# Kernel tuning notes

Measured on AMD Instinct MI355X. Metric: run time of the kernel, lower is better.

Reference implementation:

```python
import jax, jax.numpy as jnp
import numpy as np

CUTOFF = 5.2
BOX = 44.0
N_ATOMS = 8192

# 13 half-shifts used by the cell list (vector_index_displacement) + zero shift
HALF_SHIFTS = np.array([
    [-1, 0, 0], [-1, -1, 0], [0, -1, 0], [1, -1, 0],
    [-1, 1, -1], [0, 1, -1], [1, 1, -1], [-1, 0, -1],
    [0, 0, -1], [1, 0, -1], [-1, -1, -1], [0, -1, -1], [1, -1, -1]], dtype=np.int64)
ALL_SHIFTS = np.concatenate([np.zeros((1, 3), dtype=np.int64), HALF_SHIFTS], axis=0)  # (14,3)


def setup_inputs() -> dict:
    key = jax.random.key(0)
    k1, k2 = jax.random.split(key)
    species = jax.random.randint(k1, (1, N_ATOMS), 0, 4, dtype=jnp.int64)
    coordinates = jax.random.uniform(k2, (1, N_ATOMS, 3), dtype=jnp.float32) * BOX
    cell = jnp.eye(3, dtype=jnp.float32) * BOX
    pbc = jnp.ones((3,), dtype=bool)
    return {"species": species, "coordinates": coordinates, "cell": cell, "pbc": pbc}


def reference(species, coordinates, cell, pbc):
    # Single molecule, as asserted by the torch module.
    coords = coordinates[0]  # (N, 3)
    n = coords.shape[0]
    # map_to_central: wrap coordinates into the central cell
    frac = coords @ jnp.linalg.inv(cell)
    frac = frac - jnp.floor(frac)
    coords = frac @ cell
    # orthorhombic cell diagonal (norm of cell columns, as in _setup_variables)
    diag = jnp.linalg.norm(cell, axis=0)  # (3,)

    shifts = jnp.asarray(ALL_SHIFTS)
    pairs_list, shift_list = [], []
    cutoff2 = CUTOFF * CUTOFF
    for k in range(shifts.shape[0]):  # fixed small loop over 14 periodic shifts
        s = shifts[k]
        # delta[i, j] = r_i - r_j + s * cell_diagonal   (N, N, 3)
        delta = coords[:, None, :] - coords[None, :, :] + s.astype(coords.dtype) * diag
        d2 = jnp.sum(delta * delta, axis=-1)  # (N, N)
        mask = d2 <= cutoff2
        if k == 0:
            # within-image pairs: each unordered pair once, no self pairs
            mask = jnp.triu(mask, 1)
        i, j = jnp.nonzero(mask)  # eager: data-dependent pair count
        pairs_list.append(jnp.stack([i, j], axis=0))
        shift_list.append(jnp.broadcast_to(s, (i.shape[0], 3)))
    atom_pairs = jnp.concatenate(pairs_list, axis=1)  # (2, P)
    shift_indices = jnp.concatenate(shift_list, axis=0)  # (P, 3)
    return atom_pairs, shift_indices


if __name__ == "__main__":
    out = reference(**setup_inputs())
    print(out[0].shape, out[1].shape)
```

## Files before the change

kernel.cpp:

```cpp
#include <hip/hip_runtime.h>

#define CLD_NATOMS 8192
#define CLD_NSHIFT 14
#define CLD_NROWS (CLD_NSHIFT * CLD_NATOMS)
#define CLD_NTILE 112
#define CLD_NCELL 512
#define CLD_CAP 128
#define CLD_C2 ((float)(5.2 * 5.2))
#define CLD_R 5.35f

__device__ const int cld_shifts[CLD_NSHIFT][3] = {
    {0, 0, 0},
    {-1, 0, 0}, {-1, -1, 0}, {0, -1, 0}, {1, -1, 0},
    {-1, 1, -1}, {0, 1, -1}, {1, 1, -1}, {-1, 0, -1},
    {0, 0, -1}, {1, 0, -1}, {-1, -1, -1}, {0, -1, -1}, {1, -1, -1}};

__device__ float4 cld_pp[CLD_NATOMS];
__device__ int cld_cid[CLD_NATOMS];
__device__ float4 cld_sorted[CLD_NATOMS];
__device__ unsigned cld_cstart[CLD_NCELL + 1];
__device__ unsigned cld_cfill[CLD_NCELL];
__device__ int cld_jbuf[(size_t)CLD_NROWS * CLD_CAP];
__device__ unsigned cld_cnt[CLD_NROWS];
__device__ unsigned cld_off[CLD_NROWS];
__device__ unsigned cld_tot[CLD_NTILE];
__device__ float4 cld_dg;
__device__ float4 cld_cinv;
__device__ float4 cld_sf[CLD_NSHIFT];

__global__ __launch_bounds__(256) void cld_wrapbin(const float* __restrict__ coords,
                                                   const float* __restrict__ cell) {
  int i = blockIdx.x * blockDim.x + threadIdx.x;
  if (i >= CLD_NATOMS) return;
  float dgx = (float)sqrt((double)cell[0] * cell[0] + (double)cell[3] * cell[3] +
                          (double)cell[6] * cell[6]);
  float dgy = (float)sqrt((double)cell[1] * cell[1] + (double)cell[4] * cell[4] +
                          (double)cell[7] * cell[7]);
  float dgz = (float)sqrt((double)cell[2] * cell[2] + (double)cell[5] * cell[5] +
                          (double)cell[8] * cell[8]);
  float cix = 8.0f / dgx, ciy = 8.0f / dgy, ciz = 8.0f / dgz;
  if (i == 0) {
    cld_dg = make_float4(dgx, dgy, dgz, 0.f);
    cld_cinv = make_float4(cix, ciy, ciz, 0.f);
    for (int k = 0; k < CLD_NSHIFT; ++k)
      cld_sf[k] = make_float4(__fmul_rn((float)cld_shifts[k][0], dgx),
                              __fmul_rn((float)cld_shifts[k][1], dgy),
                              __fmul_rn((float)cld_shifts[k][2], dgz), 0.f);
  }

  double a00 = cell[0], a01 = cell[1], a02 = cell[2];
  double a10 = cell[3], a11 = cell[4], a12 = cell[5];
  double a20 = cell[6], a21 = cell[7], a22 = cell[8];
  double det = a00 * (a11 * a22 - a12 * a21) - a01 * (a10 * a22 - a12 * a20) +
               a02 * (a10 * a21 - a11 * a20);
  double id = 1.0 / det;
  float inv[3][3];
  inv[0][0] = (float)((a11 * a22 - a12 * a21) * id);
  inv[0][1] = (float)(-(a01 * a22 - a02 * a21) * id);
  inv[0][2] = (float)((a01 * a12 - a02 * a11) * id);
  inv[1][0] = (float)(-(a10 * a22 - a12 * a20) * id);
  inv[1][1] = (float)((a00 * a22 - a02 * a20) * id);
  inv[1][2] = (float)(-(a00 * a12 - a02 * a10) * id);
  inv[2][0] = (float)((a10 * a21 - a11 * a20) * id);
  inv[2][1] = (float)(-(a00 * a21 - a01 * a20) * id);
  inv[2][2] = (float)((a00 * a11 - a01 * a10) * id);

  float x = coords[3 * i], y = coords[3 * i + 1], z = coords[3 * i + 2];
  float fr[3], w[3];
#pragma unroll
  for (int c = 0; c < 3; ++c) {
    float f = __fadd_rn(__fadd_rn(__fmul_rn(x, inv[0][c]), __fmul_rn(y, inv[1][c])),
                        __fmul_rn(z, inv[2][c]));
    fr[c] = __fsub_rn(f, floorf(f));
  }
#pragma unroll
  for (int c = 0; c < 3; ++c) {
    w[c] = __fadd_rn(
        __fadd_rn(__fmul_rn(fr[0], cell[0 * 3 + c]), __fmul_rn(fr[1], cell[1 * 3 + c])),
        __fmul_rn(fr[2], cell[2 * 3 + c]));
  }
  cld_pp[i] = make_float4(w[0], w[1], w[2], 0.0f);
  int cx = min(7, (int)(w[0] * cix));
  int cy = min(7, (int)(w[1] * ciy));
  int cz = min(7, (int)(w[2] * ciz));
  cld_cid[i] = (cz * 8 + cy) * 8 + cx;
}

__global__ __launch_bounds__(1024) void cld_cscan() {
  __shared__ unsigned h[CLD_NCELL];
  int t = threadIdx.x;
  if (t < CLD_NCELL) h[t] = 0u;
  __syncthreads();
#pragma unroll
  for (int r = 0; r < 8; ++r) atomicAdd(&h[cld_cid[t + r * 1024]], 1u);
  __syncthreads();
  unsigned v = (t < CLD_NCELL) ? h[t] : 0u;
  unsigned acc = v;
  for (int off = 1; off < CLD_NCELL; off <<= 1) {
    unsigned a = (t >= off && t < CLD_NCELL) ? h[t - off] : 0u;
    __syncthreads();
    if (t < CLD_NCELL) {
      acc += a;
      h[t] = acc;
    }
    __syncthreads();
  }
  if (t < CLD_NCELL) {
    cld_cstart[t] = acc - v;
    cld_cfill[t] = acc - v;
  }
  if (t == CLD_NCELL - 1) cld_cstart[CLD_NCELL] = acc;
}

__global__ __launch_bounds__(256) void cld_scatter() {
  int i = blockIdx.x * blockDim.x + threadIdx.x;
  if (i >= CLD_NATOMS) return;
  unsigned pos = atomicAdd(&cld_cfill[cld_cid[i]], 1u);
  float4 p = cld_pp[i];
  p.w = __int_as_float(i);
  cld_sorted[pos] = p;
}

__device__ __forceinline__ bool cld_alive(float xi, float yi, float zi, int sx, int sy,
                                          int sz, float dgx, float dgy, float dgz) {
  bool a = true;
  if (sx < 0) a = a && (xi >= dgx - 5.3f); else if (sx > 0) a = a && (xi <= 5.3f);
  if (sy < 0) a = a && (yi >= dgy - 5.3f); else if (sy > 0) a = a && (yi <= 5.3f);
  if (sz < 0) a = a && (zi >= dgz - 5.3f); else if (sz > 0) a = a && (zi <= 5.3f);
  return a;
}

__device__ __forceinline__ void cld_crange(float t, float ci, int& lo, int& hi) {
  lo = max(0, (int)(fmaxf(t - CLD_R, 0.f) * ci));
  hi = min(7, (int)(fmaxf(t + CLD_R, 0.f) * ci));
}

__device__ __forceinline__ unsigned cld_iscan(unsigned v, int lane) {
  for (int off = 1; off < 64; off <<= 1) {
    unsigned t = __shfl_up(v, off);
    if (lane >= off) v += t;
  }
  return v;
}

__global__ __launch_bounds__(512) void cld_count() {
  __shared__ uint4 smask[8][64];
  int wslot = threadIdx.x >> 6;
  int wv = blockIdx.x * 8 + wslot;
  int lane = threadIdx.x & 63;
  unsigned* lm = (unsigned*)smask[wslot];
  int k = wv >> 13, i = wv & (CLD_NATOMS - 1);

  float4 dg = cld_dg;
  float4 sc = cld_sf[k];
  int sx = cld_shifts[k][0], sy = cld_shifts[k][1], sz = cld_shifts[k][2];
  float4 pi = cld_pp[i];
  if (k != 0 && !cld_alive(pi.x, pi.y, pi.z, sx, sy, sz, dg.x, dg.y, dg.z)) {
    if (lane == 0) cld_cnt[wv] = 0u;
    return;
  }
  smask[wslot][lane] = make_uint4(0u, 0u, 0u, 0u);

  float4 cinv = cld_cinv;
  int xlo, xhi, ylo, yhi, zlo, zhi;
  cld_crange(__fadd_rn(pi.x, sc.x), cinv.x, xlo, xhi);
  cld_crange(__fadd_rn(pi.y, sc.y), cinv.y, ylo, yhi);
  cld_crange(__fadd_rn(pi.z, sc.z), cinv.z, zlo, zhi);

  for (int cz = zlo; cz <= zhi; ++cz) {
    for (int cy = ylo; cy <= yhi; ++cy) {
      int idb = (cz * 8 + cy) * 8;
      unsigned b = cld_cstart[idb + xlo], e = cld_cstart[idb + xhi + 1];
      for (unsigned t = b + lane; t < e; t += 64) {
        float4 pj = cld_sorted[t];
        int j = __float_as_int(pj.w);
        float dx = __fadd_rn(__fsub_rn(pi.x, pj.x), sc.x);
        float dy = __fadd_rn(__fsub_rn(pi.y, pj.y), sc.y);
        float dz = __fadd_rn(__fsub_rn(pi.z, pj.z), sc.z);
        float d2 = __fadd_rn(__fadd_rn(__fmul_rn(dx, dx), __fmul_rn(dy, dy)),
                             __fmul_rn(dz, dz));
        bool ok = (d2 <= CLD_C2) && (k != 0 || i < j);
        if (ok) atomicOr(&lm[(unsigned)j >> 5], 1u << (j & 31));
      }
    }
  }
  __threadfence_block();

  const unsigned long long* mrow = (const unsigned long long*)lm;
  unsigned long long m0 = mrow[lane];
  unsigned long long m1 = mrow[64 + lane];
  unsigned c0 = (unsigned)__popcll(m0), c1 = (unsigned)__popcll(m1);
  unsigned s0 = cld_iscan(c0, lane);
  unsigned T0 = __shfl(s0, 63);
  unsigned e0 = s0 - c0;
  unsigned s1 = cld_iscan(c1, lane);
  unsigned T1 = __shfl(s1, 63);
  unsigned e1 = T0 + s1 - c1;

  size_t jb = (size_t)wv * CLD_CAP;
  unsigned p = e0;
  unsigned long long m = m0;
  while (m) {
    int b = __ffsll((long long)m) - 1;
    m &= m - 1;
    if (p < CLD_CAP) cld_jbuf[jb + p] = (lane << 6) + b;
    ++p;
  }
  p = e1;
  m = m1;
  while (m) {
    int b = __ffsll((long long)m) - 1;
    m &= m - 1;
    if (p < CLD_CAP) cld_jbuf[jb + p] = ((64 + lane) << 6) + b;
    ++p;
  }
  if (lane == 0) cld_cnt[wv] = min(T0 + T1, (unsigned)CLD_CAP);
}

__global__ __launch_bounds__(1024) void cld_s1() {
  __shared__ unsigned sd[1024];
  int t = threadIdx.x;
  int gid = blockIdx.x * 1024 + t;
  unsigned v = cld_cnt[gid];
  sd[t] = v;
  __syncthreads();
  unsigned acc = v;
  for (int off = 1; off < 1024; off <<= 1) {
    unsigned a = (t >= off) ? sd[t - off] : 0u;
    __syncthreads();
    acc += a;
    sd[t] = acc;
    __syncthreads();
  }
  cld_off[gid] = acc - v;
  if (t == 1023) cld_tot[blockIdx.x] = acc;
}

__global__ __launch_bounds__(512) void cld_emit(int* __restrict__ out, int P) {
  int wv = blockIdx.x * 8 + (threadIdx.x >> 6);
  int lane = threadIdx.x & 63;
  unsigned c = cld_cnt[wv];
  if (c == 0) return;
  int tile = wv >> 10;
  unsigned v = 0;
  if (lane < tile) v = cld_tot[lane];
  if (64 + lane < tile) v += cld_tot[64 + lane];
#pragma unroll
  for (int off = 32; off; off >>= 1) v += __shfl_down(v, off);
  unsigned tbase = __shfl(v, 0);

  unsigned off0 = cld_off[wv] + tbase;
  int k = wv >> 13, i = wv & (CLD_NATOMS - 1);
  int sx = cld_shifts[k][0], sy = cld_shifts[k][1], sz = cld_shifts[k][2];
  size_t jb = (size_t)wv * CLD_CAP;
  for (unsigned q = lane; q < c; q += 64) {
    unsigned p = off0 + q;
    if (p < (unsigned)P) {
      out[p] = i;
      out[P + p] = cld_jbuf[jb + q];
      unsigned sp = 2u * (unsigned)P + 3u * p;
      out[sp] = sx;
      out[sp + 1] = sy;
      out[sp + 2] = sz;
    }
  }
}

extern "C" void kernel_launch(void* const* d_in, const int* in_sizes, int n_in,
                              void* d_out, int out_size, void* d_ws, size_t ws_size,
                              hipStream_t stream) {
  const float* coords = (const float*)d_in[1];
  const float* cell = (const float*)d_in[2];
  int P = out_size / 5;

  cld_wrapbin<<<CLD_NATOMS / 256, 256, 0, stream>>>(coords, cell);
  cld_cscan<<<1, 1024, 0, stream>>>();
  cld_scatter<<<CLD_NATOMS / 256, 256, 0, stream>>>();
  cld_count<<<CLD_NROWS / 8, 512, 0, stream>>>();
  cld_s1<<<CLD_NTILE, 1024, 0, stream>>>();
  cld_emit<<<CLD_NROWS / 8, 512, 0, stream>>>((int*)d_out, P);
}
```

Measured before the change: 53.24 us.

## Fuse count, scan and emit into one decoupled-lookback kernel and merge cell scan with scatter

Reduces the six-launch pipeline to three. The cell histogram/scan now runs in block 0 of the scatter kernel while the other blocks spin on a flag. Count, offset scan and emit are merged into one kernel that handles 128 rows per block and obtains its global base by spinning on earlier tiles' published totals. This removes launch gaps and the global cnt/off round trips, but relies on all earlier blocks making forward progress, and the serial lookback over up to 896 tiles adds latency.

```diff
diff --git a/kernel.cpp b/kernel.cpp
--- a/kernel.cpp
+++ b/kernel.cpp
@@ -1,37 +1,62 @@
 #include <hip/hip_runtime.h>
 
-#define CLD_NATOMS 8192
-#define CLD_NSHIFT 14
-#define CLD_NROWS (CLD_NSHIFT * CLD_NATOMS)
-#define CLD_NTILE 112
-#define CLD_NCELL 512
-#define CLD_CAP 128
-#define CLD_C2 ((float)(5.2 * 5.2))
-#define CLD_R 5.35f
-
-__device__ const int cld_shifts[CLD_NSHIFT][3] = {
+#define CLH_NATOMS 8192
+#define CLH_NSHIFT 14
+#define CLH_NROWS (CLH_NSHIFT * CLH_NATOMS)
+#define CLH_NCELL 512
+#define CLH_CAP 128
+#define CLH_TROWS 128
+#define CLH_NTILE (CLH_NROWS / CLH_TROWS)
+#define CLH_C2 ((float)(5.2 * 5.2))
+#define CLH_R 5.35f
+
+__device__ const int clh_shifts[CLH_NSHIFT][3] = {
     {0, 0, 0},
     {-1, 0, 0}, {-1, -1, 0}, {0, -1, 0}, {1, -1, 0},
     {-1, 1, -1}, {0, 1, -1}, {1, 1, -1}, {-1, 0, -1},
     {0, 0, -1}, {1, 0, -1}, {-1, -1, -1}, {0, -1, -1}, {1, -1, -1}};
 
-__device__ float4 cld_pp[CLD_NATOMS];
-__device__ int cld_cid[CLD_NATOMS];
-__device__ float4 cld_sorted[CLD_NATOMS];
-__device__ unsigned cld_cstart[CLD_NCELL + 1];
-__device__ unsigned cld_cfill[CLD_NCELL];
-__device__ int cld_jbuf[(size_t)CLD_NROWS * CLD_CAP];
-__device__ unsigned cld_cnt[CLD_NROWS];
-__device__ unsigned cld_off[CLD_NROWS];
-__device__ unsigned cld_tot[CLD_NTILE];
-__device__ float4 cld_dg;
-__device__ float4 cld_cinv;
-__device__ float4 cld_sf[CLD_NSHIFT];
-
-__global__ __launch_bounds__(256) void cld_wrapbin(const float* __restrict__ coords,
+__device__ float4 clh_pp[CLH_NATOMS];
+__device__ int clh_cid[CLH_NATOMS];
+__device__ float4 clh_sorted[CLH_NATOMS];
+__device__ unsigned clh_cstart[CLH_NCELL + 1];
+__device__ unsigned clh_cfill[CLH_NCELL];
+__device__ unsigned clh_flag;
+__device__ unsigned long long clh_tstat[CLH_NTILE];
+__device__ int clh_jbuf[(size_t)CLH_NROWS * CLH_CAP];
+__device__ float4 clh_dg;
+__device__ float4 clh_cinv;
+__device__ float4 clh_sf[CLH_NSHIFT];
+
+__device__ __forceinline__ bool clh_alive(float xi, float yi, float zi, int sx, int sy,
+                                          int sz, float dgx, float dgy, float dgz) {
+  bool a = true;
+  if (sx < 0) a = a && (xi >= dgx - 5.3f); else if (sx > 0) a = a && (xi <= 5.3f);
+  if (sy < 0) a = a && (yi >= dgy - 5.3f); else if (sy > 0) a = a && (yi <= 5.3f);
+  if (sz < 0) a = a && (zi >= dgz - 5.3f); else if (sz > 0) a = a && (zi <= 5.3f);
+  return a;
+}
+
+__device__ __forceinline__ void clh_crange(float t, float ci, int& lo, int& hi) {
+  lo = max(0, (int)(fmaxf(t - CLH_R, 0.f) * ci));
+  hi = min(7, (int)(fmaxf(t + CLH_R, 0.f) * ci));
+}
+
+__device__ __forceinline__ unsigned clh_iscan(unsigned v, int lane) {
+  for (int off = 1; off < 64; off <<= 1) {
+    unsigned t = __shfl_up(v, off);
+    if (lane >= off) v += t;
+  }
+  return v;
+}
+
+__global__ __launch_bounds__(256) void clh_wrapbin(const float* __restrict__ coords,
                                                    const float* __restrict__ cell) {
   int i = blockIdx.x * blockDim.x + threadIdx.x;
-  if (i >= CLD_NATOMS) return;
+  if (i >= CLH_NATOMS) return;
+  if (i < CLH_NTILE) clh_tstat[i] = 0ull;
+  if (i == 0) clh_flag = 0u;
+
   float dgx = (float)sqrt((double)cell[0] * cell[0] + (double)cell[3] * cell[3] +
                           (double)cell[6] * cell[6]);
   float dgy = (float)sqrt((double)cell[1] * cell[1] + (double)cell[4] * cell[4] +
@@ -40,12 +65,12 @@
                           (double)cell[8] * cell[8]);
   float cix = 8.0f / dgx, ciy = 8.0f / dgy, ciz = 8.0f / dgz;
   if (i == 0) {
-    cld_dg = make_float4(dgx, dgy, dgz, 0.f);
-    cld_cinv = make_float4(cix, ciy, ciz, 0.f);
-    for (int k = 0; k < CLD_NSHIFT; ++k)
-      cld_sf[k] = make_float4(__fmul_rn((float)cld_shifts[k][0], dgx),
-                              __fmul_rn((float)cld_shifts[k][1], dgy),
-                              __fmul_rn((float)cld_shifts[k][2], dgz), 0.f);
+    clh_dg = make_float4(dgx, dgy, dgz, 0.f);
+    clh_cinv = make_float4(cix, ciy, ciz, 0.f);
+    for (int k = 0; k < CLH_NSHIFT; ++k)
+      clh_sf[k] = make_float4(__fmul_rn((float)clh_shifts[k][0], dgx),
+                              __fmul_rn((float)clh_shifts[k][1], dgy),
+                              __fmul_rn((float)clh_shifts[k][2], dgz), 0.f);
   }
 
   double a00 = cell[0], a01 = cell[1], a02 = cell[2];
@@ -79,189 +104,188 @@
         __fadd_rn(__fmul_rn(fr[0], cell[0 * 3 + c]), __fmul_rn(fr[1], cell[1 * 3 + c])),
         __fmul_rn(fr[2], cell[2 * 3 + c]));
   }
-  cld_pp[i] = make_float4(w[0], w[1], w[2], 0.0f);
+  clh_pp[i] = make_float4(w[0], w[1], w[2], 0.0f);
   int cx = min(7, (int)(w[0] * cix));
   int cy = min(7, (int)(w[1] * ciy));
   int cz = min(7, (int)(w[2] * ciz));
-  cld_cid[i] = (cz * 8 + cy) * 8 + cx;
-}
-
-__global__ __launch_bounds__(1024) void cld_cscan() {
-  __shared__ unsigned h[CLD_NCELL];
-  int t = threadIdx.x;
-  if (t < CLD_NCELL) h[t] = 0u;
+  clh_cid[i] = (cz * 8 + cy) * 8 + cx;
+}
+
+__global__ __launch_bounds__(512) void clh_scatterfused() {
+  __shared__ unsigned h[CLH_NCELL];
+  int tid = threadIdx.x;
+  if (blockIdx.x == 0) {
+    h[tid] = 0u;
+    __syncthreads();
+    for (int r = tid; r < CLH_NATOMS; r += 512) atomicAdd(&h[clh_cid[r]], 1u);
+    __syncthreads();
+    unsigned v = h[tid];
+    unsigned acc = v;
+    for (int off = 1; off < CLH_NCELL; off <<= 1) {
+      unsigned a = (tid >= off) ? h[tid - off] : 0u;
+      __syncthreads();
+      acc += a;
+      h[tid] = acc;
+      __syncthreads();
+    }
+    clh_cstart[tid] = acc - v;
+    atomicExch(&clh_cfill[tid], acc - v);
+    if (tid == CLH_NCELL - 1) clh_cstart[CLH_NCELL] = acc;
+    __threadfence();
+    __syncthreads();
+    if (tid == 0) atomicExch(&clh_flag, 1u);
+  } else {
+    if (tid == 0) {
+      while (atomicAdd(&clh_flag, 0u) == 0u) __builtin_amdgcn_s_sleep(8);
+    }
+    __syncthreads();
+    __threadfence();
+  }
+  int i = blockIdx.x * 512 + tid;
+  float4 p = clh_pp[i];
+  unsigned pos = atomicAdd(&clh_cfill[clh_cid[i]], 1u);
+  p.w = __int_as_float(i);
+  clh_sorted[pos] = p;
+}
+
+__global__ __launch_bounds__(512) void clh_mega(int* __restrict__ out, int P) {
+  __shared__ uint4 smask[8][64];
+  __shared__ unsigned scnt[CLH_TROWS];
+  __shared__ unsigned soff[CLH_TROWS];
+  __shared__ unsigned sbase;
+  int tid = threadIdx.x;
+  int wslot = tid >> 6;
+  int lane = tid & 63;
+  unsigned* lm = (unsigned*)smask[wslot];
+
+  float4 dg = clh_dg;
+  float4 cinv = clh_cinv;
+
+  for (int r = 0; r < CLH_TROWS / 8; ++r) {
+    int local = wslot * (CLH_TROWS / 8) + r;
+    int row = blockIdx.x * CLH_TROWS + local;
+    int k = row >> 13, i = row & (CLH_NATOMS - 1);
+    int sx = clh_shifts[k][0], sy = clh_shifts[k][1], sz = clh_shifts[k][2];
+    float4 pi = clh_pp[i];
+    if (k != 0 && !clh_alive(pi.x, pi.y, pi.z, sx, sy, sz, dg.x, dg.y, dg.z)) {
+      if (lane == 0) scnt[local] = 0u;
+      continue;
+    }
+    float4 sc = clh_sf[k];
+    smask[wslot][lane] = make_uint4(0u, 0u, 0u, 0u);
+
+    int xlo, xhi, ylo, yhi, zlo, zhi;
+    clh_crange(__fadd_rn(pi.x, sc.x), cinv.x, xlo, xhi);
+    clh_crange(__fadd_rn(pi.y, sc.y), cinv.y, ylo, yhi);
+    clh_crange(__fadd_rn(pi.z, sc.z), cinv.z, zlo, zhi);
+
+    for (int cz = zlo; cz <= zhi; ++cz) {
+      for (int cy = ylo; cy <= yhi; ++cy) {
+        int idb = (cz * 8 + cy) * 8;
+        unsigned b = clh_cstart[idb + xlo], e = clh_cstart[idb + xhi + 1];
+        for (unsigned t = b + lane; t < e; t += 64) {
+          float4 pj = clh_sorted[t];
+          int j = __float_as_int(pj.w);
+          float dx = __fadd_rn(__fsub_rn(pi.x, pj.x), sc.x);
+          float dy = __fadd_rn(__fsub_rn(pi.y, pj.y), sc.y);
+          float dz = __fadd_rn(__fsub_rn(pi.z, pj.z), sc.z);
+          float d2 = __fadd_rn(__fadd_rn(__fmul_rn(dx, dx), __fmul_rn(dy, dy)),
+                               __fmul_rn(dz, dz));
+          bool ok = (d2 <= CLH_C2) && (k != 0 || i < j);
+          if (ok) atomicOr(&lm[(unsigned)j >> 5], 1u << (j & 31));
+        }
+      }
+    }
+    __threadfence_block();
+
+    const unsigned long long* mrow = (const unsigned long long*)lm;
+    unsigned long long m0 = mrow[lane];
+    unsigned long long m1 = mrow[64 + lane];
+    if (__ballot((m0 | m1) != 0ull) == 0ull) {
+      if (lane == 0) scnt[local] = 0u;
+      continue;
+    }
+    unsigned c0 = (unsigned)__popcll(m0), c1 = (unsigned)__popcll(m1);
+    unsigned s0 = clh_iscan(c0, lane);
+    unsigned T0 = __shfl(s0, 63);
+    unsigned e0 = s0 - c0;
+    unsigned s1 = clh_iscan(c1, lane);
+    unsigned T1 = __shfl(s1, 63);
+    unsigned e1 = T0 + s1 - c1;
+
+    size_t jb = (size_t)row * CLH_CAP;
+    unsigned p = e0;
+    unsigned long long m = m0;
+    while (m) {
+      int b = __ffsll((long long)m) - 1;
+      m &= m - 1;
+      if (p < CLH_CAP) clh_jbuf[jb + p] = (lane << 6) + b;
+      ++p;
+    }
+    p = e1;
+    m = m1;
+    while (m) {
+      int b = __ffsll((long long)m) - 1;
+      m &= m - 1;
+      if (p < CLH_CAP) clh_jbuf[jb + p] = ((64 + lane) << 6) + b;
+      ++p;
+    }
+    if (lane == 0) scnt[local] = min(T0 + T1, (unsigned)CLH_CAP);
+  }
   __syncthreads();
-#pragma unroll
-  for (int r = 0; r < 8; ++r) atomicAdd(&h[cld_cid[t + r * 1024]], 1u);
-  __syncthreads();
-  unsigned v = (t < CLD_NCELL) ? h[t] : 0u;
-  unsigned acc = v;
-  for (int off = 1; off < CLD_NCELL; off <<= 1) {
-    unsigned a = (t >= off && t < CLD_NCELL) ? h[t - off] : 0u;
-    __syncthreads();
-    if (t < CLD_NCELL) {
-      acc += a;
-      h[t] = acc;
-    }
-    __syncthreads();
-  }
-  if (t < CLD_NCELL) {
-    cld_cstart[t] = acc - v;
-    cld_cfill[t] = acc - v;
-  }
-  if (t == CLD_NCELL - 1) cld_cstart[CLD_NCELL] = acc;
-}
-
-__global__ __launch_bounds__(256) void cld_scatter() {
-  int i = blockIdx.x * blockDim.x + threadIdx.x;
-  if (i >= CLD_NATOMS) return;
-  unsigned pos = atomicAdd(&cld_cfill[cld_cid[i]], 1u);
-  float4 p = cld_pp[i];
-  p.w = __int_as_float(i);
-  cld_sorted[pos] = p;
-}
-
-__device__ __forceinline__ bool cld_alive(float xi, float yi, float zi, int sx, int sy,
-                                          int sz, float dgx, float dgy, float dgz) {
-  bool a = true;
-  if (sx < 0) a = a && (xi >= dgx - 5.3f); else if (sx > 0) a = a && (xi <= 5.3f);
-  if (sy < 0) a = a && (yi >= dgy - 5.3f); else if (sy > 0) a = a && (yi <= 5.3f);
-  if (sz < 0) a = a && (zi >= dgz - 5.3f); else if (sz > 0) a = a && (zi <= 5.3f);
-  return a;
-}
-
-__device__ __forceinline__ void cld_crange(float t, float ci, int& lo, int& hi) {
-  lo = max(0, (int)(fmaxf(t - CLD_R, 0.f) * ci));
-  hi = min(7, (int)(fmaxf(t + CLD_R, 0.f) * ci));
-}
-
-__device__ __forceinline__ unsigned cld_iscan(unsigned v, int lane) {
-  for (int off = 1; off < 64; off <<= 1) {
-    unsigned t = __shfl_up(v, off);
-    if (lane >= off) v += t;
-  }
-  return v;
-}
-
-__global__ __launch_bounds__(512) void cld_count() {
-  __shared__ uint4 smask[8][64];
-  int wslot = threadIdx.x >> 6;
-  int wv = blockIdx.x * 8 + wslot;
-  int lane = threadIdx.x & 63;
-  unsigned* lm = (unsigned*)smask[wslot];
-  int k = wv >> 13, i = wv & (CLD_NATOMS - 1);
-
-  float4 dg = cld_dg;
-  float4 sc = cld_sf[k];
-  int sx = cld_shifts[k][0], sy = cld_shifts[k][1], sz = cld_shifts[k][2];
-  float4 pi = cld_pp[i];
-  if (k != 0 && !cld_alive(pi.x, pi.y, pi.z, sx, sy, sz, dg.x, dg.y, dg.z)) {
-    if (lane == 0) cld_cnt[wv] = 0u;
-    return;
-  }
-  smask[wslot][lane] = make_uint4(0u, 0u, 0u, 0u);
-
-  float4 cinv = cld_cinv;
-  int xlo, xhi, ylo, yhi, zlo, zhi;
-  cld_crange(__fadd_rn(pi.x, sc.x), cinv.x, xlo, xhi);
-  cld_crange(__fadd_rn(pi.y, sc.y), cinv.y, ylo, yhi);
-  cld_crange(__fadd_rn(pi.z, sc.z), cinv.z, zlo, zhi);
-
-  for (int cz = zlo; cz <= zhi; ++cz) {
-    for (int cy = ylo; cy <= yhi; ++cy) {
-      int idb = (cz * 8 + cy) * 8;
-      unsigned b = cld_cstart[idb + xlo], e = cld_cstart[idb + xhi + 1];
-      for (unsigned t = b + lane; t < e; t += 64) {
-        float4 pj = cld_sorted[t];
-        int j = __float_as_int(pj.w);
-        float dx = __fadd_rn(__fsub_rn(pi.x, pj.x), sc.x);
-        float dy = __fadd_rn(__fsub_rn(pi.y, pj.y), sc.y);
-        float dz = __fadd_rn(__fsub_rn(pi.z, pj.z), sc.z);
-        float d2 = __fadd_rn(__fadd_rn(__fmul_rn(dx, dx), __fmul_rn(dy, dy)),
-                             __fmul_rn(dz, dz));
-        bool ok = (d2 <= CLD_C2) && (k != 0 || i < j);
-        if (ok) atomicOr(&lm[(unsigned)j >> 5], 1u << (j & 31));
-      }
-    }
-  }
-  __threadfence_block();
-
-  const unsigned long long* mrow = (const unsigned long long*)lm;
-  unsigned long long m0 = mrow[lane];
-  unsigned long long m1 = mrow[64 + lane];
-  unsigned c0 = (unsigned)__popcll(m0), c1 = (unsigned)__popcll(m1);
-  unsigned s0 = cld_iscan(c0, lane);
-  unsigned T0 = __shfl(s0, 63);
-  unsigned e0 = s0 - c0;
-  unsigned s1 = cld_iscan(c1, lane);
-  unsigned T1 = __shfl(s1, 63);
-  unsigned e1 = T0 + s1 - c1;
-
-  size_t jb = (size_t)wv * CLD_CAP;
-  unsigned p = e0;
-  unsigned long long m = m0;
-  while (m) {
-    int b = __ffsll((long long)m) - 1;
-    m &= m - 1;
-    if (p < CLD_CAP) cld_jbuf[jb + p] = (lane << 6) + b;
-    ++p;
-  }
-  p = e1;
-  m = m1;
-  while (m) {
-    int b = __ffsll((long long)m) - 1;
-    m &= m - 1;
-    if (p < CLD_CAP) cld_jbuf[jb + p] = ((64 + lane) << 6) + b;
-    ++p;
-  }
-  if (lane == 0) cld_cnt[wv] = min(T0 + T1, (unsigned)CLD_CAP);
-}
-
-__global__ __launch_bounds__(1024) void cld_s1() {
-  __shared__ unsigned sd[1024];
-  int t = threadIdx.x;
-  int gid = blockIdx.x * 1024 + t;
-  unsigned v = cld_cnt[gid];
-  sd[t] = v;
+
+  unsigned v = (tid < CLH_TROWS) ? scnt[tid] : 0u;
+  if (tid < CLH_TROWS) soff[tid] = v;
   __syncthreads();
   unsigned acc = v;
-  for (int off = 1; off < 1024; off <<= 1) {
-    unsigned a = (t >= off) ? sd[t - off] : 0u;
-    __syncthreads();
-    acc += a;
-    sd[t] = acc;
-    __syncthreads();
-  }
-  cld_off[gid] = acc - v;
-  if (t == 1023) cld_tot[blockIdx.x] = acc;
-}
-
-__global__ __launch_bounds__(512) void cld_emit(int* __restrict__ out, int P) {
-  int wv = blockIdx.x * 8 + (threadIdx.x >> 6);
-  int lane = threadIdx.x & 63;
-  unsigned c = cld_cnt[wv];
-  if (c == 0) return;
-  int tile = wv >> 10;
-  unsigned v = 0;
-  if (lane < tile) v = cld_tot[lane];
-  if (64 + lane < tile) v += cld_tot[64 + lane];
+  for (int off = 1; off < CLH_TROWS; off <<= 1) {
+    unsigned a = (tid >= off && tid < CLH_TROWS) ? soff[tid - off] : 0u;
+    __syncthreads();
+    if (tid < CLH_TROWS) {
+      acc += a;
+      soff[tid] = acc;
+    }
+    __syncthreads();
+  }
+  if (tid == 0)
+    atomicExch(&clh_tstat[blockIdx.x],
+               (1ull << 32) | (unsigned long long)soff[CLH_TROWS - 1]);
+  if (tid < 64) {
+    unsigned sum = 0;
+    for (int t = tid; t < (int)blockIdx.x; t += 64) {
+      unsigned long long vv;
+      do {
+        vv = atomicAdd(&clh_tstat[t], 0ull);
+        if (!(vv >> 32)) __builtin_amdgcn_s_sleep(2);
+      } while (!(vv >> 32));
+      sum += (unsigned)vv;
+    }
 #pragma unroll
-  for (int off = 32; off; off >>= 1) v += __shfl_down(v, off);
-  unsigned tbase = __shfl(v, 0);
-
-  unsigned off0 = cld_off[wv] + tbase;
-  int k = wv >> 13, i = wv & (CLD_NATOMS - 1);
-  int sx = cld_shifts[k][0], sy = cld_shifts[k][1], sz = cld_shifts[k][2];
-  size_t jb = (size_t)wv * CLD_CAP;
-  for (unsigned q = lane; q < c; q += 64) {
-    unsigned p = off0 + q;
-    if (p < (unsigned)P) {
-      out[p] = i;
-      out[P + p] = cld_jbuf[jb + q];
-      unsigned sp = 2u * (unsigned)P + 3u * p;
-      out[sp] = sx;
-      out[sp + 1] = sy;
-      out[sp + 2] = sz;
+    for (int off = 32; off; off >>= 1) sum += __shfl_down(sum, off);
+    if (tid == 0) sbase = sum;
+  }
+  __syncthreads();
+
+  unsigned tbase = sbase;
+  for (int r = 0; r < CLH_TROWS / 8; ++r) {
+    int local = wslot * (CLH_TROWS / 8) + r;
+    unsigned c = scnt[local];
+    if (c == 0) continue;
+    int row = blockIdx.x * CLH_TROWS + local;
+    int k = row >> 13, i = row & (CLH_NATOMS - 1);
+    int sx = clh_shifts[k][0], sy = clh_shifts[k][1], sz = clh_shifts[k][2];
+    unsigned off0 = tbase + soff[local] - c;
+    size_t jb = (size_t)row * CLH_CAP;
+    for (unsigned q = lane; q < c; q += 64) {
+      unsigned p = off0 + q;
+      if (p < (unsigned)P) {
+        out[p] = i;
+        out[P + p] = clh_jbuf[jb + q];
+        unsigned sp = 2u * (unsigned)P + 3u * p;
+        out[sp] = sx;
+        out[sp + 1] = sy;
+        out[sp + 2] = sz;
+      }
     }
   }
 }
@@ -273,10 +297,7 @@
   const float* cell = (const float*)d_in[2];
   int P = out_size / 5;
 
-  cld_wrapbin<<<CLD_NATOMS / 256, 256, 0, stream>>>(coords, cell);
-  cld_cscan<<<1, 1024, 0, stream>>>();
-  cld_scatter<<<CLD_NATOMS / 256, 256, 0, stream>>>();
-  cld_count<<<CLD_NROWS / 8, 512, 0, stream>>>();
-  cld_s1<<<CLD_NTILE, 1024, 0, stream>>>();
-  cld_emit<<<CLD_NROWS / 8, 512, 0, stream>>>((int*)d_out, P);
-}
+  clh_wrapbin<<<CLH_NATOMS / 256, 256, 0, stream>>>(coords, cell);
+  clh_scatterfused<<<16, 512, 0, stream>>>();
+  clh_mega<<<CLH_NTILE, 512, 0, stream>>>((int*)d_out, P);
+}
```

Result: slower. 117.7 us (+121.1%).
